# Performance work log

Hardware: AMD Instinct MI355X
Metric: run time of the kernel (lower is better)

## Reference

```python
import jax, jax.numpy as jnp
import numpy as np

N = 1000; K = 500; M = N - K          # codeword / info / parity bits
NUE = 4; NBS = 4                      # tx / rx antennas
BPS = 4; RATE = 0.5; NSYM = N // BPS  # 16-QAM, 250 symbols per codeword
NITER = 5                             # BP iterations

# 16-QAM constellation, Gray-coded per axis (Sionna-style), unit energy
_bits = ((np.arange(16)[:, None] >> np.array([3, 2, 1, 0])) & 1).astype(np.float32)
_re = (1 - 2 * _bits[:, 0]) * (2 - (1 - 2 * _bits[:, 2]))
_im = (1 - 2 * _bits[:, 1]) * (2 - (1 - 2 * _bits[:, 3]))
POINTS = jnp.asarray((_re + 1j * _im) / np.sqrt(10.0), dtype=jnp.complex64)  # [16]
LABELS = jnp.asarray(_bits)  # [16,4] bit labels per point


def setup_inputs() -> dict:
    key = jax.random.key(0)
    ks = jax.random.split(key, 5)
    batch = 1000
    # systematic sparse LDPC-like code: H = [P^T | I_M], info-bit degree 3
    rs = np.random.RandomState(0)
    P = np.zeros((K, M), np.int32)
    for i in range(K):
        P[i, rs.choice(M, 3, replace=False)] = 1
    vi, ci = np.nonzero(P)
    vn = np.concatenate([vi, K + np.arange(M)]).astype(np.int32)  # [2000]
    cn = np.concatenate([ci, np.arange(M)]).astype(np.int32)      # [2000]
    b = jax.random.randint(ks[0], (batch, NUE, K), 0, 2, dtype=jnp.int32)
    h_re = jax.random.normal(ks[1], (batch * NSYM, NBS, NUE), jnp.float32)
    h_im = jax.random.normal(ks[2], (batch * NSYM, NBS, NUE), jnp.float32)
    n_re = jax.random.normal(ks[3], (batch * NSYM, NBS), jnp.float32)
    n_im = jax.random.normal(ks[4], (batch * NSYM, NBS), jnp.float32)
    return {"batch_size": batch, "ebno_db": jnp.full((1,), 5.0, jnp.float32),
            "b": b, "P": jnp.asarray(P), "cn_idx": jnp.asarray(cn),
            "vn_idx": jnp.asarray(vn), "h_re": h_re, "h_im": h_im,
            "noise_re": n_re, "noise_im": n_im}


def _forward(batch_size, ebno_db, b, P, cn_idx, vn_idx, h_re, h_im, noise_re, noise_im):
    no = 1.0 / (10.0 ** (ebno_db[0] / 10.0) * BPS * RATE)  # ebnodb2no
    # --- LDPC encode (systematic): c = [b, b@P mod 2] ---
    bf = b.astype(jnp.float32)
    parity = jnp.mod(jnp.round(bf @ P.astype(jnp.float32)), 2.0)
    c = jnp.concatenate([bf, parity], -1)                    # [B,NUE,N]
    # --- QAM mapper ---
    idx = (c.reshape(batch_size, NUE, NSYM, BPS) @ jnp.array([8., 4., 2., 1.], jnp.float32)).astype(jnp.int32)
    x = POINTS[idx]                                          # [B,NUE,NSYM]
    x_f = jnp.transpose(x, (0, 2, 1)).reshape(-1, NUE)       # [B*NSYM,NUE]
    # --- flat fading channel, h ~ CN(0,1), AWGN ---
    h = ((h_re + 1j * h_im) / np.sqrt(2.0)).astype(jnp.complex64)
    w = ((noise_re + 1j * noise_im) * jnp.sqrt(no / 2.0)).astype(jnp.complex64)
    y = jnp.einsum('bij,bj->bi', h, x_f) + w                 # [B*NSYM,NBS]
    # --- LMMSE equalizer: G = H^H (H H^H + no I)^-1, unbiased scaling ---
    A = jnp.einsum('bik,bjk->bij', h, jnp.conj(h)) \
        + no.astype(jnp.complex64) * jnp.eye(NBS, dtype=jnp.complex64)
    Ainv_y = jnp.linalg.solve(A, y[..., None])[..., 0]
    x_raw = jnp.einsum('bij,bi->bj', jnp.conj(h), Ainv_y)    # G y, [B*NSYM,NUE]
    GH = jnp.einsum('bij,bik->bjk', jnp.conj(h), jnp.linalg.solve(A, h))
    d = jnp.real(jnp.diagonal(GH, axis1=1, axis2=2))         # diag(GH), [B*NSYM,NUE]
    x_hat = x_raw / d.astype(jnp.complex64)
    no_eff = jnp.maximum(1.0 / d - 1.0, 1e-12)
    x_hat = jnp.transpose(x_hat.reshape(batch_size, NSYM, NUE), (0, 2, 1))  # [B,NUE,NSYM]
    nvar = jnp.transpose(no_eff.reshape(batch_size, NSYM, NUE), (0, 2, 1))
    # --- max-log demapper, L = log p(b=0)/p(b=1) ---
    metric = -(jnp.abs(x_hat[..., None] - POINTS) ** 2) / nvar[..., None]   # [B,NUE,NSYM,16]
    NEG = jnp.float32(-1e30)
    m5 = metric[..., None, :]                               # [B,NUE,NSYM,1,16]
    lab = LABELS.T[None, None, None]                        # [1,1,1,4,16]
    m0 = jnp.max(jnp.where(lab == 0, m5, NEG), -1)
    m1 = jnp.max(jnp.where(lab == 1, m5, NEG), -1)
    llr = (m0 - m1).reshape(batch_size, NUE, N)
    # --- LDPC BP decoder (sum-product over fixed sparse Tanner graph) ---
    Lch = llr.reshape(batch_size * NUE, N).T                # [N, Bc]
    c2v = jnp.zeros((cn_idx.shape[0], Lch.shape[1]), jnp.float32)  # [E, Bc]
    for _ in range(NITER):
        vtot = Lch.at[vn_idx].add(c2v)                      # Lch + segment_sum(c2v)
        m_vc = vtot[vn_idx] - c2v                           # extrinsic VN->CN
        t = jnp.tanh(jnp.clip(m_vc * 0.5, -9.9, 9.9))
        t = jnp.where(t >= 0, jnp.maximum(t, 1e-7), jnp.minimum(t, -1e-7))
        prod = jax.ops.segment_prod(t, cn_idx, num_segments=M)
        c2v = 2.0 * jnp.arctanh(jnp.clip(prod[cn_idx] / t, -0.999999, 0.999999))
    vtot = Lch.at[vn_idx].add(c2v)
    b_hat = (vtot[:K].T < 0).astype(jnp.float32).reshape(batch_size, NUE, K)
    return bf, b_hat


def reference(batch_size, ebno_db, b, P, cn_idx, vn_idx, h_re, h_im, noise_re, noise_im):
    return _forward(batch_size, ebno_db, b, P, cn_idx, vn_idx,
                    h_re, h_im, noise_re, noise_im)
```

## Files before the change

kernel.cpp:

```cpp
#include <hip/hip_runtime.h>
#include <math.h>

#define KK     500
#define MM     500
#define NNODES 1000
#define NSYM   250
#define NITERS 5
#define MAXVDEG 4
#define EMAX   2048
#define TB     256

__global__ void __launch_bounds__(512)
k_setup(const int* __restrict__ cn, const int* __restrict__ vn, int E,
        const float* __restrict__ ebno, const int* __restrict__ P,
        const int* __restrict__ b, int ncw,
        int* __restrict__ cinfo, int* __restrict__ vlist, int* __restrict__ coff,
        double* __restrict__ nobuf, unsigned* __restrict__ Ppack,
        unsigned* __restrict__ bpack, float* __restrict__ out, int packBlocks) {
  __shared__ int sdeg[512];
  __shared__ int ssc[512];
  __shared__ int scur[512];
  __shared__ int svc[NNODES];
  int tid = threadIdx.x;
  int bx = blockIdx.x;

  if (bx == 0) {
    sdeg[tid] = 0;
    for (int n = tid; n < NNODES; n += 512) svc[n] = 0;
    __syncthreads();
    for (int e = tid; e < E; e += 512) atomicAdd(&sdeg[cn[e]], 1);
    __syncthreads();
    int v = sdeg[tid];
    ssc[tid] = v;
    __syncthreads();
    for (int o = 1; o < 512; o <<= 1) {
      int x = (tid >= o) ? ssc[tid - o] : 0;
      __syncthreads();
      ssc[tid] += x;
      __syncthreads();
    }
    int excl = ssc[tid] - v;
    scur[tid] = excl;
    if (tid < MM) {
      coff[tid] = excl;
      if (tid == MM - 1) coff[MM] = ssc[tid];
    }
    __syncthreads();
    for (int e = tid; e < E; e += 512) {
      int c = cn[e], n = vn[e];
      int slot;
      if (n >= KK) {
        slot = ssc[c] - 1;
      } else {
        slot = atomicAdd(&scur[c], 1);
      }
      cinfo[slot] = (c << 16) | n;
      if (n < KK) {
        int t = atomicAdd(&svc[n], 1);
        if (t < MAXVDEG) vlist[n * MAXVDEG + t] = slot;
      }
    }
    if (tid == 0) {
      double no = 1.0 / (pow(10.0, (double)ebno[0] * 0.1) * 2.0);
      nobuf[0] = no;
      nobuf[1] = sqrt(no * 0.5);
    }
    return;
  }

  if (bx <= packBlocks) {
    int id = (bx - 1) * 512 + tid;
    if (id < MM * 16) {
      int j = id >> 4, w = id & 15;
      unsigned word = 0u;
      int base = w * 32;
      for (int bit = 0; bit < 32; ++bit) {
        int i = base + bit;
        if (i < KK && P[i * MM + j] != 0) word |= (1u << bit);
      }
      Ppack[j * 16 + w] = word;
    } else {
      int id2 = id - MM * 16;
      if (id2 < ncw * 16) {
        int cw = id2 >> 4, w = id2 & 15;
        unsigned word = 0u;
        int base = w * 32;
        for (int bit = 0; bit < 32; ++bit) {
          int i = base + bit;
          if (i < KK && b[cw * KK + i] != 0) word |= (1u << bit);
        }
        bpack[cw * 16 + w] = word;
      }
    }
    return;
  }

  int id = (bx - 1 - packBlocks) * 512 + tid;
  if (id < ncw * KK) out[id] = (float)b[id];
}

__device__ __forceinline__ void qam_pointf(int p, float& re, float& im) {
  const float s = 0.31622776601683794f;
  int b0 = (p >> 3) & 1, b1 = (p >> 2) & 1, b2 = (p >> 1) & 1, b3 = p & 1;
  re = (float)((1 - 2 * b0) * (2 - (1 - 2 * b2))) * s;
  im = (float)((1 - 2 * b1) * (2 - (1 - 2 * b3))) * s;
}

__device__ __forceinline__ float tanh_half(float m) {
  float mc = fminf(fmaxf(m, -19.8f), 19.8f);
  float e = __expf(mc);
  float t = 1.0f - __fdividef(2.0f, e + 1.0f);
  return (t >= 0.0f) ? fmaxf(t, 1e-7f) : fminf(t, -1e-7f);
}
__device__ __forceinline__ float pclip(float P, float t) {
  return copysignf(fminf(fabsf(P), 0.999999f * fabsf(t)), P);
}
__device__ __forceinline__ float tfloor(float t) {
  return (t >= 0.0f) ? fmaxf(t, 1e-7f) : fminf(t, -1e-7f);
}
__device__ __forceinline__ float atanh2c(float P, float t) {
  float r = __fdividef(P, t);
  r = fminf(fmaxf(r, -0.999999f), 0.999999f);
  return __logf(__fdividef(1.0f + r, 1.0f - r));
}

#define SOLVE_DEMAP(J, Lout) {                                                          \
  float u0r = Hr[0][J] * i00,               u0i = Hi[0][J] * i00;                       \
  float u1r = (Hr[1][J] - (L10r * u0r - L10i * u0i)) * i11;                             \
  float u1i = (Hi[1][J] - (L10r * u0i + L10i * u0r)) * i11;                             \
  float u2r = (Hr[2][J] - (L20r * u0r - L20i * u0i) - (L21r * u1r - L21i * u1i)) * i22; \
  float u2i = (Hi[2][J] - (L20r * u0i + L20i * u0r) - (L21r * u1i + L21i * u1r)) * i22; \
  float u3r = (Hr[3][J] - (L30r * u0r - L30i * u0i) - (L31r * u1r - L31i * u1i)         \
                        - (L32r * u2r - L32i * u2i)) * i33;                             \
  float u3i = (Hi[3][J] - (L30r * u0i + L30i * u0r) - (L31r * u1i + L31i * u1r)         \
                        - (L32r * u2i + L32i * u2r)) * i33;                             \
  float dj = (u0r * u0r + u0i * u0i) + (u1r * u1r + u1i * u1i)                          \
           + (u2r * u2r + u2i * u2i) + (u3r * u3r + u3i * u3i);                         \
  float rr = (u0r * yr[0] + u0i * yi[0]) + (u1r * yr[1] + u1i * yi[1])                  \
           + (u2r * yr[2] + u2i * yi[2]) + (u3r * yr[3] + u3i * yi[3]);                 \
  float ri = (u0r * yi[0] - u0i * yr[0]) + (u1r * yi[1] - u1i * yr[1])                  \
           + (u2r * yi[2] - u2i * yr[2]) + (u3r * yi[3] - u3i * yr[3]);                 \
  float rdj = __fdividef(1.0f, dj);                                                    \
  float xhr = rr * rdj, xhi = ri * rdj;                                                \
  float gap = 1.0f - dj;                                                               \
  float inoe = __fdividef(dj, fmaxf(gap, dj * 1e-12f));                                \
  float m0[4] = {-1e30f, -1e30f, -1e30f, -1e30f};                                      \
  float m1[4] = {-1e30f, -1e30f, -1e30f, -1e30f};                                      \
  _Pragma("unroll")                                                                    \
  for (int p = 0; p < 16; ++p) {                                                       \
    float dr = xhr - PRT[p], di = xhi - PIT[p];                                        \
    float met = -(dr * dr + di * di) * inoe;                                           \
    _Pragma("unroll")                                                                  \
    for (int k = 0; k < 4; ++k) {                                                      \
      if ((p >> (3 - k)) & 1) m1[k] = fmaxf(m1[k], met);                               \
      else                    m0[k] = fmaxf(m0[k], met);                               \
    }                                                                                  \
  }                                                                                    \
  _Pragma("unroll")                                                                    \
  for (int k = 0; k < 4; ++k) Lout[k] = m0[k] - m1[k];                                 \
}

__global__ void __launch_bounds__(256, 4)
k_fused(const float* __restrict__ h_re, const float* __restrict__ h_im,
        const float* __restrict__ n_re, const float* __restrict__ n_im,
        const double* __restrict__ nobuf,
        const unsigned* __restrict__ bpack, const unsigned* __restrict__ Ppack,
        const int* __restrict__ vlist, const int* __restrict__ coff,
        const int* __restrict__ cinfo, float* __restrict__ out, int ncw) {
  __shared__ float2 sT[EMAX];
  __shared__ float2 sP[512];
  __shared__ float2 sL[NNODES];

  int tid = threadIdx.x;
  int pairId = blockIdx.x;
  int bt = pairId >> 1, plane = pairId & 1;

  if (tid < NSYM) {
    int t = bt * NSYM + tid;
    int s = tid;

    float no = (float)nobuf[0];
    float sq = (float)nobuf[1];
    const float is2 = 0.70710678118654752f;

    float Hr[4][4], Hi[4][4];
    {
      const float4* hr4 = (const float4*)h_re;
      const float4* hi4 = (const float4*)h_im;
      #pragma unroll
      for (int i = 0; i < 4; ++i) {
        float4 a = hr4[t * 4 + i], c = hi4[t * 4 + i];
        Hr[i][0] = a.x * is2; Hr[i][1] = a.y * is2;
        Hr[i][2] = a.z * is2; Hr[i][3] = a.w * is2;
        Hi[i][0] = c.x * is2; Hi[i][1] = c.y * is2;
        Hi[i][2] = c.z * is2; Hi[i][3] = c.w * is2;
      }
    }

    float xr[4], xi[4];
    #pragma unroll
    for (int ue = 0; ue < 4; ++ue) {
      const unsigned* bp = bpack + (bt * 4 + ue) * 16;
      int v = 0;
      #pragma unroll
      for (int k = 0; k < 4; ++k) {
        int n = 4 * s + k;
        int bit;
        if (n < KK) {
          bit = (bp[n >> 5] >> (n & 31)) & 1;
        } else {
          const unsigned* pp = Ppack + (n - KK) * 16;
          int cnt = 0;
          #pragma unroll
          for (int w = 0; w < 16; ++w) cnt += __popc(bp[w] & pp[w]);
          bit = cnt & 1;
        }
        v = (v << 1) | bit;
      }
      qam_pointf(v, xr[ue], xi[ue]);
    }

    float yr[4], yi[4];
    {
      float4 wr = ((const float4*)n_re)[t];
      float4 wi = ((const float4*)n_im)[t];
      float wrv[4] = {wr.x, wr.y, wr.z, wr.w};
      float wiv[4] = {wi.x, wi.y, wi.z, wi.w};
      #pragma unroll
      for (int i = 0; i < 4; ++i) {
        float ar = wrv[i] * sq;
        float ai = wiv[i] * sq;
        #pragma unroll
        for (int j = 0; j < 4; ++j) {
          ar += Hr[i][j] * xr[j] - Hi[i][j] * xi[j];
          ai += Hr[i][j] * xi[j] + Hi[i][j] * xr[j];
        }
        yr[i] = ar; yi[i] = ai;
      }
    }

    auto dotc = [&](int i, int j, float& ar, float& ai) {
      float r = 0.0f, m = 0.0f;
      #pragma unroll
      for (int k = 0; k < 4; ++k) {
        r += Hr[i][k] * Hr[j][k] + Hi[i][k] * Hi[j][k];
        m += Hi[i][k] * Hr[j][k] - Hr[i][k] * Hi[j][k];
      }
      ar = r; ai = m;
    };
    float a00, a11, a22, a33, dum;
    float a10r, a10i, a20r, a20i, a21r, a21i, a30r, a30i, a31r, a31i, a32r, a32i;
    dotc(0, 0, a00, dum);  a00 += no;
    dotc(1, 0, a10r, a10i);
    dotc(1, 1, a11, dum);  a11 += no;
    dotc(2, 0, a20r, a20i);
    dotc(2, 1, a21r, a21i);
    dotc(2, 2, a22, dum);  a22 += no;
    dotc(3, 0, a30r, a30i);
    dotc(3, 1, a31r, a31i);
    dotc(3, 2, a32r, a32i);
    dotc(3, 3, a33, dum);  a33 += no;

    float i00 = rsqrtf(a00);
    float L10r = a10r * i00, L10i = a10i * i00;
    float L20r = a20r * i00, L20i = a20i * i00;
    float L30r = a30r * i00, L30i = a30i * i00;
    float d11 = a11 - (L10r * L10r + L10i * L10i);
    float i11 = rsqrtf(d11);
    float L21r = (a21r - (L20r * L10r + L20i * L10i)) * i11;
    float L21i = (a21i - (L20i * L10r - L20r * L10i)) * i11;
    float L31r = (a31r - (L30r * L10r + L30i * L10i)) * i11;
    float L31i = (a31i - (L30i * L10r - L30r * L10i)) * i11;
    float d22 = a22 - (L20r * L20r + L20i * L20i) - (L21r * L21r + L21i * L21i);
    float i22 = rsqrtf(d22);
    float L32r = (a32r - (L30r * L20r + L30i * L20i) - (L31r * L21r + L31i * L21i)) * i22;
    float L32i = (a32i - (L30i * L20r - L30r * L20i) - (L31i * L21r - L31r * L21i)) * i22;
    float d33 = a33 - (L30r * L30r + L30i * L30i) - (L31r * L31r + L31i * L31i)
                    - (L32r * L32r + L32i * L32i);
    float i33 = rsqrtf(d33);

    {
      float v0r = yr[0] * i00,               v0i = yi[0] * i00;
      float v1r = (yr[1] - (L10r * v0r - L10i * v0i)) * i11;
      float v1i = (yi[1] - (L10r * v0i + L10i * v0r)) * i11;
      float v2r = (yr[2] - (L20r * v0r - L20i * v0i) - (L21r * v1r - L21i * v1i)) * i22;
      float v2i = (yi[2] - (L20r * v0i + L20i * v0r) - (L21r * v1i + L21i * v1r)) * i22;
      float v3r = (yr[3] - (L30r * v0r - L30i * v0i) - (L31r * v1r - L31i * v1i)
                         - (L32r * v2r - L32i * v2i)) * i33;
      float v3i = (yi[3] - (L30r * v0i + L30i * v0r) - (L31r * v1i + L31i * v1r)
                         - (L32r * v2i + L32i * v2r)) * i33;
      yr[0] = v0r; yi[0] = v0i; yr[1] = v1r; yi[1] = v1i;
      yr[2] = v2r; yi[2] = v2i; yr[3] = v3r; yi[3] = v3i;
    }

    const float PRT[16] = { 0.31622776601683794f, 0.31622776601683794f, 0.9486832980505138f, 0.9486832980505138f,
                            0.31622776601683794f, 0.31622776601683794f, 0.9486832980505138f, 0.9486832980505138f,
                           -0.31622776601683794f,-0.31622776601683794f,-0.9486832980505138f,-0.9486832980505138f,
                           -0.31622776601683794f,-0.31622776601683794f,-0.9486832980505138f,-0.9486832980505138f };
    const float PIT[16] = { 0.31622776601683794f, 0.9486832980505138f, 0.31622776601683794f, 0.9486832980505138f,
                           -0.31622776601683794f,-0.9486832980505138f,-0.31622776601683794f,-0.9486832980505138f,
                            0.31622776601683794f, 0.9486832980505138f, 0.31622776601683794f, 0.9486832980505138f,
                           -0.31622776601683794f,-0.9486832980505138f,-0.31622776601683794f,-0.9486832980505138f };

    float lA[4], lB[4];
    if (plane == 0) {
      SOLVE_DEMAP(0, lA);
      SOLVE_DEMAP(1, lB);
    } else {
      SOLVE_DEMAP(2, lA);
      SOLVE_DEMAP(3, lB);
    }
    #pragma unroll
    for (int k = 0; k < 4; ++k) {
      sL[4 * s + k] = make_float2(lA[k], lB[k]);
    }
  }
  __syncthreads();

  float2 Ln[2], En[2];
  int pk0[2], pk1[2], pk2[2]; bool iok[2];
  #pragma unroll
  for (int i = 0; i < 2; ++i) {
    int n = tid + TB * i;
    iok[i] = n < KK;
    Ln[i] = make_float2(0.f, 0.f);
    En[i] = make_float2(1.f, 1.f);
    pk0[i] = pk1[i] = pk2[i] = 0;
    if (iok[i]) {
      float2 L = sL[n];
      Ln[i] = L;
      En[i] = make_float2(__expf(fminf(fmaxf(L.x, -55.f), 55.f)),
                          __expf(fminf(fmaxf(L.y, -55.f), 55.f)));
      int s0 = vlist[n * MAXVDEG], s1 = vlist[n * MAXVDEG + 1], s2 = vlist[n * MAXVDEG + 2];
      pk0[i] = (cinfo[s0] & 0xffff0000) | s0;
      pk1[i] = (cinfo[s1] & 0xffff0000) | s1;
      pk2[i] = (cinfo[s2] & 0xffff0000) | s2;
    }
  }
  float2 qpar0, qpar1;
  {
    float2 Lp0 = sL[KK + tid];
    qpar0 = make_float2(tanh_half(Lp0.x), tanh_half(Lp0.y));
  }
  bool c1ok = (tid + TB) < MM;
  if (c1ok) {
    float2 Lp1 = sL[KK + tid + TB];
    qpar1 = make_float2(tanh_half(Lp1.x), tanh_half(Lp1.y));
  } else {
    qpar1 = make_float2(1.f, 1.f);
  }
  int beg0 = coff[tid], end0 = coff[tid + 1];
  int beg1 = c1ok ? coff[tid + TB] : 0;
  int end1 = c1ok ? coff[tid + TB + 1] : 0;

  for (int it = 0; it < NITERS; ++it) {
    if (it == 0) {
      #pragma unroll
      for (int i = 0; i < 2; ++i) {
        if (iok[i]) {
          float2 t = make_float2(tanh_half(Ln[i].x), tanh_half(Ln[i].y));
          sT[pk0[i] & 0xffff] = t;
          sT[pk1[i] & 0xffff] = t;
          sT[pk2[i] & 0xffff] = t;
        }
      }
    } else {
      #pragma unroll
      for (int i = 0; i < 2; ++i) {
        if (iok[i]) {
          int s0 = pk0[i] & 0xffff, c0 = ((unsigned)pk0[i]) >> 16;
          int s1 = pk1[i] & 0xffff, c1 = ((unsigned)pk1[i]) >> 16;
          int s2 = pk2[i] & 0xffff, c2 = ((unsigned)pk2[i]) >> 16;
          float2 P0 = sP[c0], P1 = sP[c1], P2 = sP[c2];
          float2 t0 = sT[s0], t1 = sT[s1], t2 = sT[s2];
          float p0 = pclip(P0.x, t0.x), p1 = pclip(P1.x, t1.x), p2 = pclip(P2.x, t2.x);
          float a0 = t0.x + p0, a1 = t1.x + p1, a2 = t2.x + p2;
          float b0 = t0.x - p0, b1 = t1.x - p1, b2 = t2.x - p2;
          float Ex = En[i].x;
          float A0 = Ex * (a1 * a2), A1 = Ex * (a0 * a2), A2 = Ex * (a0 * a1);
          float B0 = b1 * b2,        B1 = b0 * b2,        B2 = b0 * b1;
          float n0x = tfloor(__fdividef(A0 - B0, A0 + B0));
          float n1x = tfloor(__fdividef(A1 - B1, A1 + B1));
          float n2x = tfloor(__fdividef(A2 - B2, A2 + B2));
          float q0 = pclip(P0.y, t0.y), q1 = pclip(P1.y, t1.y), q2 = pclip(P2.y, t2.y);
          float c0a = t0.y + q0, c1a = t1.y + q1, c2a = t2.y + q2;
          float d0b = t0.y - q0, d1b = t1.y - q1, d2b = t2.y - q2;
          float Ey = En[i].y;
          float C0 = Ey * (c1a * c2a), C1 = Ey * (c0a * c2a), C2 = Ey * (c0a * c1a);
          float D0 = d1b * d2b,        D1 = d0b * d2b,        D2 = d0b * d1b;
          float n0y = tfloor(__fdividef(C0 - D0, C0 + D0));
          float n1y = tfloor(__fdividef(C1 - D1, C1 + D1));
          float n2y = tfloor(__fdividef(C2 - D2, C2 + D2));
          sT[s0] = make_float2(n0x, n0y);
          sT[s1] = make_float2(n1x, n1y);
          sT[s2] = make_float2(n2x, n2y);
        }
      }
    }
    __syncthreads();
    {
      float px = qpar0.x, py = qpar0.y;
      for (int e = beg0; e < end0 - 1; ++e) { float2 tt = sT[e]; px *= tt.x; py *= tt.y; }
      sP[tid] = make_float2(px, py);
      if (c1ok) {
        float qx = qpar1.x, qy = qpar1.y;
        for (int e = beg1; e < end1 - 1; ++e) { float2 tt = sT[e]; qx *= tt.x; qy *= tt.y; }
        sP[tid + TB] = make_float2(qx, qy);
      }
    }
    __syncthreads();
  }

  int cw0 = pairId * 2;
  float* o0 = out + (size_t)ncw * KK + (size_t)cw0 * KK;
  float* o1 = o0 + KK;
  #pragma unroll
  for (int i = 0; i < 2; ++i) {
    if (iok[i]) {
      int n = tid + TB * i;
      int s0 = pk0[i] & 0xffff, c0 = ((unsigned)pk0[i]) >> 16;
      int s1 = pk1[i] & 0xffff, c1 = ((unsigned)pk1[i]) >> 16;
      int s2 = pk2[i] & 0xffff, c2 = ((unsigned)pk2[i]) >> 16;
      float2 P0 = sP[c0], P1 = sP[c1], P2 = sP[c2];
      float2 t0 = sT[s0], t1 = sT[s1], t2 = sT[s2];
      float2 L = Ln[i];
      float ax = L.x + atanh2c(P0.x, t0.x) + atanh2c(P1.x, t1.x) + atanh2c(P2.x, t2.x);
      float ay = L.y + atanh2c(P0.y, t0.y) + atanh2c(P1.y, t1.y) + atanh2c(P2.y, t2.y);
      o0[n] = (ax < 0.0f) ? 1.0f : 0.0f;
      o1[n] = (ay < 0.0f) ? 1.0f : 0.0f;
    }
  }
}

extern "C" void kernel_launch(void* const* d_in, const int* in_sizes, int n_in,
                              void* d_out, int out_size, void* d_ws, size_t ws_size,
                              hipStream_t stream) {
  const float* ebno = (const float*)d_in[1];
  const int*   b    = (const int*)d_in[2];
  const int*   P    = (const int*)d_in[3];
  const int*   cn   = (const int*)d_in[4];
  const int*   vn   = (const int*)d_in[5];
  const float* h_re = (const float*)d_in[6];
  const float* h_im = (const float*)d_in[7];
  const float* nre  = (const float*)d_in[8];
  const float* nim  = (const float*)d_in[9];
  float* out = (float*)d_out;

  int E     = in_sizes[4];
  int batch = in_sizes[2] / (4 * KK);
  int ncw   = batch * 4;

  char* ws = (char*)d_ws;
  size_t off = 0;
  auto alloc = [&](size_t bytes) -> void* {
    void* p = ws + off;
    off += (bytes + 255) & ~(size_t)255;
    return p;
  };
  unsigned* Ppack  = (unsigned*)alloc((size_t)MM * 16 * 4);
  unsigned* bpack  = (unsigned*)alloc((size_t)ncw * 16 * 4);
  int*      coff   = (int*)alloc((size_t)(MM + 1) * 4);
  int*      cinfo  = (int*)alloc((size_t)EMAX * 4);
  int*      vlist  = (int*)alloc((size_t)NNODES * MAXVDEG * 4);
  double*   nobuf  = (double*)alloc(2 * 8);
  (void)ws_size; (void)n_in; (void)out_size;

  int packItems  = MM * 16 + ncw * 16;
  int packBlocks = (packItems + 511) / 512;
  int bfBlocks   = (ncw * KK + 511) / 512;
  int setupGrid  = 1 + packBlocks + bfBlocks;

  k_setup<<<dim3(setupGrid), dim3(512), 0, stream>>>(cn, vn, E, ebno, P, b, ncw,
                                                     cinfo, vlist, coff, nobuf,
                                                     Ppack, bpack, out, packBlocks);
  k_fused<<<dim3(ncw / 2), dim3(256), 0, stream>>>(h_re, h_im, nre, nim, nobuf,
                                                   bpack, Ppack, vlist, coff, cinfo,
                                                   out, ncw);
}
```

Before: 178.6 us.

## Sort check nodes by degree, pad edge slots, alias LLR buffer onto edge buffer

```diff
diff --git a/kernel.cpp b/kernel.cpp
--- a/kernel.cpp
+++ b/kernel.cpp
@@ -7,7 +7,7 @@
 #define NSYM   250
 #define NITERS 5
 #define MAXVDEG 4
-#define EMAX   2048
+#define EMAX   2560
 #define TB     256
 
 __global__ void __launch_bounds__(512)
@@ -15,22 +15,46 @@
         const float* __restrict__ ebno, const int* __restrict__ P,
         const int* __restrict__ b, int ncw,
         int* __restrict__ cinfo, int* __restrict__ vlist, int* __restrict__ coff,
+        int* __restrict__ cdend, int* __restrict__ cperm,
         double* __restrict__ nobuf, unsigned* __restrict__ Ppack,
         unsigned* __restrict__ bpack, float* __restrict__ out, int packBlocks) {
   __shared__ int sdeg[512];
+  __shared__ int scinv[512];
+  __shared__ int srlen[512];
+  __shared__ int sdnew[512];
+  __shared__ int sexcl[512];
   __shared__ int ssc[512];
   __shared__ int scur[512];
   __shared__ int svc[NNODES];
+  __shared__ int shist[64];
+  __shared__ int shcur[64];
   int tid = threadIdx.x;
   int bx = blockIdx.x;
 
   if (bx == 0) {
     sdeg[tid] = 0;
     for (int n = tid; n < NNODES; n += 512) svc[n] = 0;
+    if (tid < 64) { shist[tid] = 0; shcur[tid] = 0; }
     __syncthreads();
     for (int e = tid; e < E; e += 512) atomicAdd(&sdeg[cn[e]], 1);
     __syncthreads();
-    int v = sdeg[tid];
+    int d = (tid < MM) ? sdeg[tid] : 0;
+    if (tid < MM) atomicAdd(&shist[d], 1);
+    __syncthreads();
+    if (tid == 0) {
+      int acc = 0;
+      for (int i = 0; i < 64; ++i) { int h = shist[i]; shist[i] = acc; shcur[i] = acc; acc += h; }
+    }
+    __syncthreads();
+    if (tid < MM) {
+      int nid = atomicAdd(&shcur[d], 1);
+      scinv[tid] = nid;
+      cperm[nid] = tid;
+      sdnew[nid] = d;
+      srlen[nid] = d + ((d & 1) ^ 1);
+    }
+    __syncthreads();
+    int v = (tid < MM) ? srlen[tid] : 0;
     ssc[tid] = v;
     __syncthreads();
     for (int o = 1; o < 512; o <<= 1) {
@@ -40,21 +64,24 @@
       __syncthreads();
     }
     int excl = ssc[tid] - v;
+    sexcl[tid] = excl;
     scur[tid] = excl;
     if (tid < MM) {
-      coff[tid] = excl;
+      coff[tid]  = excl;
+      cdend[tid] = excl + sdnew[tid] - 1;
       if (tid == MM - 1) coff[MM] = ssc[tid];
     }
     __syncthreads();
     for (int e = tid; e < E; e += 512) {
       int c = cn[e], n = vn[e];
+      int nc = scinv[c];
       int slot;
       if (n >= KK) {
-        slot = ssc[c] - 1;
+        slot = sexcl[nc] + sdeg[c] - 1;
       } else {
-        slot = atomicAdd(&scur[c], 1);
-      }
-      cinfo[slot] = (c << 16) | n;
+        slot = atomicAdd(&scur[nc], 1);
+      }
+      cinfo[slot] = (nc << 16) | n;
       if (n < KK) {
         int t = atomicAdd(&svc[n], 1);
         if (t < MAXVDEG) vlist[n * MAXVDEG + t] = slot;
@@ -166,10 +193,11 @@
         const double* __restrict__ nobuf,
         const unsigned* __restrict__ bpack, const unsigned* __restrict__ Ppack,
         const int* __restrict__ vlist, const int* __restrict__ coff,
+        const int* __restrict__ cdend, const int* __restrict__ cperm,
         const int* __restrict__ cinfo, float* __restrict__ out, int ncw) {
   __shared__ float2 sT[EMAX];
   __shared__ float2 sP[512];
-  __shared__ float2 sL[NNODES];
+  float2* sL = sT;
 
   int tid = threadIdx.x;
   int pairId = blockIdx.x;
@@ -339,19 +367,21 @@
   }
   float2 qpar0, qpar1;
   {
-    float2 Lp0 = sL[KK + tid];
+    int oc0 = cperm[tid];
+    float2 Lp0 = sL[KK + oc0];
     qpar0 = make_float2(tanh_half(Lp0.x), tanh_half(Lp0.y));
   }
   bool c1ok = (tid + TB) < MM;
   if (c1ok) {
-    float2 Lp1 = sL[KK + tid + TB];
+    int oc1 = cperm[tid + TB];
+    float2 Lp1 = sL[KK + oc1];
     qpar1 = make_float2(tanh_half(Lp1.x), tanh_half(Lp1.y));
   } else {
     qpar1 = make_float2(1.f, 1.f);
   }
-  int beg0 = coff[tid], end0 = coff[tid + 1];
-  int beg1 = c1ok ? coff[tid + TB] : 0;
-  int end1 = c1ok ? coff[tid + TB + 1] : 0;
+  int beg0 = coff[tid],                  dnd0 = cdend[tid];
+  int beg1 = c1ok ? coff[tid + TB]  : 0, dnd1 = c1ok ? cdend[tid + TB] : 0;
+  __syncthreads();
 
   for (int it = 0; it < NITERS; ++it) {
     if (it == 0) {
@@ -400,11 +430,11 @@
     __syncthreads();
     {
       float px = qpar0.x, py = qpar0.y;
-      for (int e = beg0; e < end0 - 1; ++e) { float2 tt = sT[e]; px *= tt.x; py *= tt.y; }
+      for (int e = beg0; e < dnd0; ++e) { float2 tt = sT[e]; px *= tt.x; py *= tt.y; }
       sP[tid] = make_float2(px, py);
       if (c1ok) {
         float qx = qpar1.x, qy = qpar1.y;
-        for (int e = beg1; e < end1 - 1; ++e) { float2 tt = sT[e]; qx *= tt.x; qy *= tt.y; }
+        for (int e = beg1; e < dnd1; ++e) { float2 tt = sT[e]; qx *= tt.x; qy *= tt.y; }
         sP[tid + TB] = make_float2(qx, qy);
       }
     }
@@ -460,6 +490,8 @@
   unsigned* Ppack  = (unsigned*)alloc((size_t)MM * 16 * 4);
   unsigned* bpack  = (unsigned*)alloc((size_t)ncw * 16 * 4);
   int*      coff   = (int*)alloc((size_t)(MM + 1) * 4);
+  int*      cdend  = (int*)alloc((size_t)MM * 4);
+  int*      cperm  = (int*)alloc((size_t)MM * 4);
   int*      cinfo  = (int*)alloc((size_t)EMAX * 4);
   int*      vlist  = (int*)alloc((size_t)NNODES * MAXVDEG * 4);
   double*   nobuf  = (double*)alloc(2 * 8);
@@ -471,9 +503,9 @@
   int setupGrid  = 1 + packBlocks + bfBlocks;
 
   k_setup<<<dim3(setupGrid), dim3(512), 0, stream>>>(cn, vn, E, ebno, P, b, ncw,
-                                                     cinfo, vlist, coff, nobuf,
-                                                     Ppack, bpack, out, packBlocks);
+                                                     cinfo, vlist, coff, cdend, cperm,
+                                                     nobuf, Ppack, bpack, out, packBlocks);
   k_fused<<<dim3(ncw / 2), dim3(256), 0, stream>>>(h_re, h_im, nre, nim, nobuf,
-                                                   bpack, Ppack, vlist, coff, cinfo,
-                                                   out, ncw);
-}
+                                                   bpack, Ppack, vlist, coff, cdend,
+                                                   cperm, cinfo, out, ncw);
+}
```

Measured after the change: 178.6 us. Within noise of the previous version (-0.0%).
